# Kernel optimization log

Hardware: AMD Instinct MI355X
Metric: run time of the kernel (lower is better)

Reference implementation:

```python
import jax, jax.numpy as jnp
import numpy as np

D = 768
N_TASKS = 4


def setup_inputs() -> dict:
    key = jax.random.key(0)
    k1, k2, k3, k4, k5 = jax.random.split(key, 5)
    b, s, t = 8, 1024, 1024
    source_features = jax.random.normal(k1, (b, s, D), dtype=jnp.float32)
    target_features = jax.random.normal(k2, (b, t, D), dtype=jnp.float32)
    # learned params: nn.Linear(768,1) + Sigmoid, nn.Embedding(4,768), alpha
    W_cost = jax.random.normal(k3, (D, 1), dtype=jnp.float32) / np.sqrt(D)
    b_cost = jnp.zeros((1,), dtype=jnp.float32)
    task_emb = jax.random.normal(k4, (N_TASKS, D), dtype=jnp.float32)
    alpha = jnp.float32(0.05)
    return {
        "source_features": source_features,
        "target_features": target_features,
        "W_cost": W_cost,
        "b_cost": b_cost,
        "task_emb": task_emb,
        "alpha": alpha,
        "task_id": 2,
    }


def reference(source_features, target_features, W_cost, b_cost, task_emb, alpha, task_id):
    # metric='cosine': elementwise cos of the raw dot-product matrix (as in source)
    dots = jnp.einsum("bsd,btd->bst", source_features, target_features)
    cost = (1.0 - jnp.cos(dots)) / 2.0  # [b,s,t]

    # use_kernel_cost=True: gaussian kernel with h = 1 * std (unbiased, over last two dims)
    std = jnp.std(cost, axis=(-1, -2), keepdims=True, ddof=1)
    cost = jnp.exp(-((cost / std) ** 2) / 2.0)

    # train_cost_matrix=True: conditional MLP on (src + tgt + task_fea), Linear(768,1)+Sigmoid.
    # Linear is applied before the nonlinearity, so decompose to avoid the [b,s,t,768] tensor.
    s_proj = jnp.einsum("bsd,d->bs", source_features, W_cost[:, 0])  # [b,s]
    t_proj = jnp.einsum("btd,d->bt", target_features, W_cost[:, 0])  # [b,t]
    task_proj = jnp.dot(task_emb[task_id], W_cost[:, 0])  # scalar
    cond = jax.nn.sigmoid(
        s_proj[:, :, None] + t_proj[:, None, :] + task_proj + b_cost[0]
    )  # [b,s,t]

    cost = alpha * (cost + cond)
    return cost
```

## Files before the change

### kernel.cpp

```cpp
#include <hip/hip_runtime.h>
#include <hip/hip_bf16.h>
#include <math.h>

#define BATCHES 8
#define SEQ 1024
#define DDIM 768
#define NPANEL 16
#define NK64 12
#define CHUNK_B 8192
#define NK32 24
#define QMAX 6.35f

typedef unsigned short u16;
typedef __attribute__((ext_vector_type(8))) short bf16x8;
typedef __attribute__((ext_vector_type(8))) unsigned short u16x8;
typedef __attribute__((ext_vector_type(4))) float f32x4;
typedef __attribute__((ext_vector_type(4))) int i32x4;

static __device__ __forceinline__ u16 f2bf(float x) {
    union { float f; unsigned u; } v; v.f = x;
    unsigned r = v.u + 0x7FFFu + ((v.u >> 16) & 1u);
    return (u16)(r >> 16);
}
static __device__ __forceinline__ float bf2f(u16 h) {
    union { float f; unsigned u; } v; v.u = ((unsigned)h) << 16; return v.f;
}

__global__ __launch_bounds__(256) void prep_i8(
    const float* __restrict__ S, const float* __restrict__ T,
    const float* __restrict__ W, const float* __restrict__ bcost,
    const float* __restrict__ temb, const int* __restrict__ task_id,
    unsigned char* __restrict__ Sg, unsigned char* __restrict__ Tg,
    float* __restrict__ sproj, float* __restrict__ tproj,
    float* __restrict__ cterm)
{
    int t = threadIdx.x;
    int g = blockIdx.x * 256 + t;
    int r  = g & 15;
    int kg = (g >> 4) & 3;
    int m  = (g >> 6) & 3;
    int x  = g >> 8;
    int ks = x % NK64;
    int y  = x / NK64;
    int p  = y & 15;
    int b  = (y >> 4) & 7;
    int tensor = y >> 7;

    int row_loc = p * 64 + m * 16 + r;
    int row_glb = b * SEQ + row_loc;
    int col = ks * 64 + kg * 16;

    const float* src = (tensor ? T : S) + (size_t)row_glb * DDIM + col;
    float4 f0 = *(const float4*)(src);
    float4 f1 = *(const float4*)(src + 4);
    float4 f2 = *(const float4*)(src + 8);
    float4 f3 = *(const float4*)(src + 12);
    float4 w0 = *(const float4*)(W + col);
    float4 w1 = *(const float4*)(W + col + 4);
    float4 w2 = *(const float4*)(W + col + 8);
    float4 w3 = *(const float4*)(W + col + 12);

    float xv[16] = {f0.x,f0.y,f0.z,f0.w, f1.x,f1.y,f1.z,f1.w,
                    f2.x,f2.y,f2.z,f2.w, f3.x,f3.y,f3.z,f3.w};
    float wv[16] = {w0.x,w0.y,w0.z,w0.w, w1.x,w1.y,w1.z,w1.w,
                    w2.x,w2.y,w2.z,w2.w, w3.x,w3.y,w3.z,w3.w};

    float pd = 0.f;
    #pragma unroll
    for (int e = 0; e < 16; ++e) pd = fmaf(xv[e], wv[e], pd);
    pd += __shfl_down(pd, 32);
    pd += __shfl_down(pd, 16);
    if ((t & 63) < 16)
        atomicAdd((tensor ? tproj : sproj) + row_glb, pd);

    const float s     = QMAX / 127.0f;
    const float inv_s = 127.0f / QMAX;
    const float inv_s2 = 252.0f / s;
    unsigned q1w[4] = {0,0,0,0}, q2w[4] = {0,0,0,0};
    #pragma unroll
    for (int e = 0; e < 16; ++e) {
        float v = xv[e];
        float q1f = rintf(v * inv_s);
        q1f = fminf(fmaxf(q1f, -127.f), 127.f);
        float rr = fmaf(-q1f, s, v);
        float q2f = rintf(rr * inv_s2);
        q2f = fminf(fmaxf(q2f, -126.f), 126.f);
        unsigned b1 = (unsigned)(unsigned char)(char)(int)q1f;
        unsigned b2 = (unsigned)(unsigned char)(char)(int)q2f;
        q1w[e >> 2] |= b1 << ((e & 3) * 8);
        q2w[e >> 2] |= b2 << ((e & 3) * 8);
    }
    unsigned char* dst = (tensor ? Tg : Sg)
        + (size_t)((b * NPANEL + p) * NK64 + ks) * CHUNK_B
        + (m * 1024 + kg * 256 + r * 16);
    *(uint4*)dst          = (uint4){q1w[0], q1w[1], q1w[2], q1w[3]};
    *(uint4*)(dst + 4096) = (uint4){q2w[0], q2w[1], q2w[2], q2w[3]};

    if (blockIdx.x == 0 && t < 64) {
        int tid = *task_id;
        float sacc = 0.f;
        #pragma unroll
        for (int d = t; d < DDIM; d += 64) sacc = fmaf(temb[tid * DDIM + d], W[d], sacc);
        #pragma unroll
        for (int o = 32; o; o >>= 1) sacc += __shfl_down(sacc, o);
        if (t == 0) *cterm = sacc + bcost[0];
    }
}

__global__ __launch_bounds__(256) void proj_kernel(
    const float* __restrict__ S, const float* __restrict__ T,
    const float* __restrict__ W, const float* __restrict__ bcost,
    const float* __restrict__ temb, const int* __restrict__ task_id,
    float* __restrict__ sproj, float* __restrict__ tproj,
    float* __restrict__ cterm)
{
    int gw   = (blockIdx.x * blockDim.x + threadIdx.x) >> 6;
    int lane = threadIdx.x & 63;

    if (gw < 2 * BATCHES * SEQ) {
        const float* rowp = (gw < BATCHES * SEQ)
            ? S + (size_t)gw * DDIM
            : T + (size_t)(gw - BATCHES * SEQ) * DDIM;
        float s = 0.f;
        #pragma unroll
        for (int d = lane; d < DDIM; d += 64) s = fmaf(rowp[d], W[d], s);
        #pragma unroll
        for (int o = 32; o; o >>= 1) s += __shfl_down(s, o);
        if (lane == 0) {
            if (gw < BATCHES * SEQ) sproj[gw] = s;
            else                    tproj[gw - BATCHES * SEQ] = s;
        }
    }
    if (blockIdx.x == gridDim.x - 1 && (threadIdx.x >> 6) == 0) {
        int tid = *task_id;
        float s = 0.f;
        #pragma unroll
        for (int d = lane; d < DDIM; d += 64) s = fmaf(temb[tid * DDIM + d], W[d], s);
        #pragma unroll
        for (int o = 32; o; o >>= 1) s += __shfl_down(s, o);
        if (lane == 0) *cterm = s + bcost[0];
    }
}

__global__ __launch_bounds__(256, 2) void gemm_i8(
    const unsigned char* __restrict__ Sg, const unsigned char* __restrict__ Tg,
    float* __restrict__ out, double* __restrict__ batch_sums)
{
    __shared__ double red[8];

    const int t    = threadIdx.x;
    const int lane = t & 63;
    const int w    = t >> 6;

    int swz  = ((blockIdx.x & 7) << 6) + (blockIdx.x >> 3);
    int tile = swz * 4 + w;
    const int b  = tile >> 8;
    const int by = (tile >> 4) & 15;
    const int bx = tile & 15;

    i32x4 acc_hh[4][4], acc_x[4][4];
    #pragma unroll
    for (int m = 0; m < 4; ++m)
        #pragma unroll
        for (int n = 0; n < 4; ++n) {
            acc_hh[m][n] = (i32x4){0,0,0,0};
            acc_x[m][n]  = (i32x4){0,0,0,0};
        }

    const unsigned char* Achunk = Sg + (size_t)((b * NPANEL + by) * NK64) * CHUNK_B + lane * 16;
    const unsigned char* Bchunk = Tg + (size_t)((b * NPANEL + bx) * NK64) * CHUNK_B + lane * 16;

    #pragma unroll 1
    for (int ks = 0; ks < NK64; ++ks) {
        const unsigned char* Ak = Achunk + (size_t)ks * CHUNK_B;
        const unsigned char* Bk = Bchunk + (size_t)ks * CHUNK_B;
        i32x4 a1[4], a2[4], b1[4], b2[4];
        #pragma unroll
        for (int m = 0; m < 4; ++m) {
            a1[m] = *(const i32x4*)(Ak + m * 1024);
            a2[m] = *(const i32x4*)(Ak + 4096 + m * 1024);
        }
        #pragma unroll
        for (int n = 0; n < 4; ++n) {
            b1[n] = *(const i32x4*)(Bk + n * 1024);
            b2[n] = *(const i32x4*)(Bk + 4096 + n * 1024);
        }
        #pragma unroll
        for (int m = 0; m < 4; ++m)
            #pragma unroll
            for (int n = 0; n < 4; ++n) {
                acc_hh[m][n] = __builtin_amdgcn_mfma_i32_16x16x64_i8(a1[m], b1[n], acc_hh[m][n], 0, 0, 0);
                acc_x[m][n]  = __builtin_amdgcn_mfma_i32_16x16x64_i8(a1[m], b2[n], acc_x[m][n], 0, 0, 0);
                acc_x[m][n]  = __builtin_amdgcn_mfma_i32_16x16x64_i8(a2[m], b1[n], acc_x[m][n], 0, 0, 0);
            }
    }

    const float S2  = (QMAX / 127.0f) * (QMAX / 127.0f);
    const float S2F = S2 / 252.0f;
    float lsum = 0.f, lsq = 0.f;
    float* outb = out + (size_t)b * SEQ * SEQ;
    const int rbase = by * 64;
    const int cbase = bx * 64;
    const int cr = lane >> 4;
    const int cc = lane & 15;
    #pragma unroll
    for (int m = 0; m < 4; ++m) {
        #pragma unroll
        for (int n = 0; n < 4; ++n) {
            int col = cbase + n * 16 + cc;
            #pragma unroll
            for (int j = 0; j < 4; ++j) {
                int row = rbase + m * 16 + cr * 4 + j;
                float d  = S2 * (float)acc_hh[m][n][j] + S2F * (float)acc_x[m][n][j];
                float c0 = 0.5f - 0.5f * __cosf(d);
                outb[(size_t)row * SEQ + col] = c0;
                lsum += c0;
                lsq  = fmaf(c0, c0, lsq);
            }
        }
    }

    double s = (double)lsum, q = (double)lsq;
    #pragma unroll
    for (int o = 32; o; o >>= 1) { s += __shfl_down(s, o); q += __shfl_down(q, o); }
    if (lane == 0) { red[w] = s; red[4 + w] = q; }
    __syncthreads();
    if (t == 0) {
        s = red[0] + red[1] + red[2] + red[3];
        q = red[4] + red[5] + red[6] + red[7];
        atomicAdd(&batch_sums[b * 2 + 0], s);
        atomicAdd(&batch_sums[b * 2 + 1], q);
    }
}

__global__ __launch_bounds__(256) void gemm_fused_bf16(
    const float* __restrict__ S, const float* __restrict__ T,
    float* __restrict__ out, double* __restrict__ batch_sums)
{
    __shared__ __align__(16) u16 lds[16384];
    __shared__ double red[8];

    const int t    = threadIdx.x;
    const int lane = t & 63;
    const int w    = t >> 6;
    const int wr   = w >> 1, wc = w & 1;

    int wg = (blockIdx.x & 7) * 64 + (blockIdx.x >> 3);
    const int b  = wg >> 6;
    const int by = (wg >> 3) & 7;
    const int bx = wg & 7;

    f32x4 acc[4][4];
    #pragma unroll
    for (int m = 0; m < 4; ++m)
        #pragma unroll
        for (int n = 0; n < 4; ++n) acc[m][n] = (f32x4){0.f, 0.f, 0.f, 0.f};

    const float* Sb = S + (size_t)b * SEQ * DDIM;
    const float* Tb = T + (size_t)b * SEQ * DDIM;
    const float* pa[2]; const float* pb[2];
    float4 ra[2][2], rb[2][2];
    #pragma unroll
    for (int i = 0; i < 2; ++i) {
        int g = t + i * 256;
        int m = g >> 6, kg = (g >> 4) & 3, r = g & 15;
        pa[i] = Sb + (size_t)(by * 128 + m * 16 + r) * DDIM + kg * 8;
        pb[i] = Tb + (size_t)(bx * 128 + m * 16 + r) * DDIM + kg * 8;
    }

    auto LOADREGS = [&](int ks) {
        #pragma unroll
        for (int i = 0; i < 2; ++i) {
            ra[i][0] = *(const float4*)(pa[i] + ks * 32);
            ra[i][1] = *(const float4*)(pa[i] + ks * 32 + 4);
            rb[i][0] = *(const float4*)(pb[i] + ks * 32);
            rb[i][1] = *(const float4*)(pb[i] + ks * 32 + 4);
        }
    };
    auto STAGE_FUSED = [&]() {
        #pragma unroll
        for (int i = 0; i < 2; ++i) {
            int g = t + i * 256;
            float xa[8] = {ra[i][0].x, ra[i][0].y, ra[i][0].z, ra[i][0].w,
                           ra[i][1].x, ra[i][1].y, ra[i][1].z, ra[i][1].w};
            float xb[8] = {rb[i][0].x, rb[i][0].y, rb[i][0].z, rb[i][0].w,
                           rb[i][1].x, rb[i][1].y, rb[i][1].z, rb[i][1].w};
            u16x8 ah, al, bh, bl;
            #pragma unroll
            for (int e = 0; e < 8; ++e) {
                u16 h = f2bf(xa[e]); ah[e] = h; al[e] = f2bf(xa[e] - bf2f(h));
                u16 g2 = f2bf(xb[e]); bh[e] = g2; bl[e] = f2bf(xb[e] - bf2f(g2));
            }
            *(u16x8*)&lds[(size_t)g * 8]         = ah;
            *(u16x8*)&lds[4096 + (size_t)g * 8]  = al;
            *(u16x8*)&lds[8192 + (size_t)g * 8]  = bh;
            *(u16x8*)&lds[12288 + (size_t)g * 8] = bl;
        }
    };
    auto COMPUTE = [&]() {
        const u16* L = &lds[0];
        bf16x8 ah[4], al[4], bh[4], bl[4];
        #pragma unroll
        for (int m = 0; m < 4; ++m) {
            int sm = wr * 4 + m;
            ah[m] = *(const bf16x8*)(L + sm * 512 + lane * 8);
            al[m] = *(const bf16x8*)(L + 4096 + sm * 512 + lane * 8);
        }
        #pragma unroll
        for (int n = 0; n < 4; ++n) {
            int sn = wc * 4 + n;
            bh[n] = *(const bf16x8*)(L + 8192 + sn * 512 + lane * 8);
            bl[n] = *(const bf16x8*)(L + 12288 + sn * 512 + lane * 8);
        }
        #pragma unroll
        for (int m = 0; m < 4; ++m)
            #pragma unroll
            for (int n = 0; n < 4; ++n) {
                acc[m][n] = __builtin_amdgcn_mfma_f32_16x16x32_bf16(ah[m], bh[n], acc[m][n], 0, 0, 0);
                acc[m][n] = __builtin_amdgcn_mfma_f32_16x16x32_bf16(ah[m], bl[n], acc[m][n], 0, 0, 0);
                acc[m][n] = __builtin_amdgcn_mfma_f32_16x16x32_bf16(al[m], bh[n], acc[m][n], 0, 0, 0);
            }
    };

    LOADREGS(0);
    for (int ks = 0; ks < NK32; ++ks) {
        STAGE_FUSED();
        __syncthreads();
        if (ks + 1 < NK32) LOADREGS(ks + 1);
        COMPUTE();
        __syncthreads();
    }

    float lsum = 0.f, lsq = 0.f;
    float* outb = out + (size_t)b * SEQ * SEQ;
    const int rbase = by * 128 + wr * 64;
    const int cbase = bx * 128 + wc * 64;
    const int cr = lane >> 4;
    const int cc = lane & 15;
    #pragma unroll
    for (int m = 0; m < 4; ++m) {
        #pragma unroll
        for (int n = 0; n < 4; ++n) {
            int col = cbase + n * 16 + cc;
            #pragma unroll
            for (int j = 0; j < 4; ++j) {
                int row = rbase + m * 16 + cr * 4 + j;
                float d  = acc[m][n][j];
                float c0 = 0.5f - 0.5f * __cosf(d);
                outb[(size_t)row * SEQ + col] = c0;
                lsum += c0;
                lsq  = fmaf(c0, c0, lsq);
            }
        }
    }

    double s = (double)lsum, q = (double)lsq;
    #pragma unroll
    for (int o = 32; o; o >>= 1) { s += __shfl_down(s, o); q += __shfl_down(q, o); }
    if (lane == 0) { red[w] = s; red[4 + w] = q; }
    __syncthreads();
    if (t == 0) {
        s = red[0] + red[1] + red[2] + red[3];
        q = red[4] + red[5] + red[6] + red[7];
        atomicAdd(&batch_sums[b * 2 + 0], s);
        atomicAdd(&batch_sums[b * 2 + 1], q);
    }
}

__global__ __launch_bounds__(256) void finalize_kernel(
    float* __restrict__ out, const double* __restrict__ batch_sums,
    const float* __restrict__ sproj, const float* __restrict__ tproj,
    const float* __restrict__ cterm_p, const float* __restrict__ alpha_p)
{
    const double n = (double)SEQ * (double)SEQ;
    size_t idx4 = (size_t)blockIdx.x * blockDim.x + threadIdx.x;
    size_t base = idx4 * 4;
    int batch = (int)(base >> 20);
    int rem   = (int)(base & ((SEQ * SEQ) - 1));
    int srow  = rem >> 10;
    int tcol  = rem & (SEQ - 1);

    double sum = batch_sums[batch * 2 + 0];
    double sq  = batch_sums[batch * 2 + 1];
    double var = (sq - sum * sum / n) / (n - 1.0);
    float inv_std = (float)(1.0 / sqrt(var));

    float alpha = *alpha_p;
    float ct    = *cterm_p;
    float sp    = sproj[batch * SEQ + srow];
    float4 tp   = *(const float4*)&tproj[batch * SEQ + tcol];
    float4 c    = *(float4*)&out[base];

    float4 r;
    { float x = c.x * inv_std; float g = __expf(-0.5f * x * x);
      float z = sp + tp.x + ct; float cd = 1.f / (1.f + __expf(-z)); r.x = alpha * (g + cd); }
    { float x = c.y * inv_std; float g = __expf(-0.5f * x * x);
      float z = sp + tp.y + ct; float cd = 1.f / (1.f + __expf(-z)); r.y = alpha * (g + cd); }
    { float x = c.z * inv_std; float g = __expf(-0.5f * x * x);
      float z = sp + tp.z + ct; float cd = 1.f / (1.f + __expf(-z)); r.z = alpha * (g + cd); }
    { float x = c.w * inv_std; float g = __expf(-0.5f * x * x);
      float z = sp + tp.w + ct; float cd = 1.f / (1.f + __expf(-z)); r.w = alpha * (g + cd); }
    *(float4*)&out[base] = r;
}

extern "C" void kernel_launch(void* const* d_in, const int* in_sizes, int n_in,
                              void* d_out, int out_size, void* d_ws, size_t ws_size,
                              hipStream_t stream) {
    const float* S      = (const float*)d_in[0];
    const float* T      = (const float*)d_in[1];
    const float* W      = (const float*)d_in[2];
    const float* bcost  = (const float*)d_in[3];
    const float* temb   = (const float*)d_in[4];
    const float* alpha  = (const float*)d_in[5];
    const int*   taskid = (const int*)d_in[6];
    float* out = (float*)d_out;

    double* batch_sums = (double*)d_ws;
    float*  sproj = (float*)((char*)d_ws + 128);
    float*  tproj = sproj + BATCHES * SEQ;
    float*  cterm = tproj + BATCHES * SEQ;

    const size_t ZERO_BYTES = 128 + sizeof(float) * (2 * BATCHES * SEQ + 1);
    const size_t SMALL = (size_t)1 << 20;
    const size_t CONV_B = (size_t)BATCHES * NPANEL * NK64 * CHUNK_B;
    const size_t NEEDED = SMALL + 2 * CONV_B;
    unsigned char* Sg = (unsigned char*)d_ws + SMALL;
    unsigned char* Tg = Sg + CONV_B;

    hipMemsetAsync(d_ws, 0, ZERO_BYTES, stream);

    if (ws_size >= NEEDED) {
        int nblk = (2 * BATCHES * NPANEL * NK64 * 256) / 256;
        prep_i8<<<nblk, 256, 0, stream>>>(S, T, W, bcost, temb, taskid,
                                          Sg, Tg, sproj, tproj, cterm);
        gemm_i8<<<512, 256, 0, stream>>>(Sg, Tg, out, batch_sums);
    } else {
        proj_kernel<<<4097, 256, 0, stream>>>(S, T, W, bcost, temb, taskid,
                                              sproj, tproj, cterm);
        gemm_fused_bf16<<<512, 256, 0, stream>>>(S, T, out, batch_sums);
    }

    int nblk2 = (BATCHES * SEQ * SEQ) / (256 * 4);
    finalize_kernel<<<nblk2, 256, 0, stream>>>(out, batch_sums, sproj, tproj,
                                               cterm, alpha);
}
```

Baseline: 66.95 us.

## Store intermediate cosine cost as fp16 and halve per-wave GEMM tile

The int8 GEMM now writes the intermediate (1-cos)/2 values to an fp16 scratch buffer instead of fp32 into the output. A new finalize kernel reads that buffer eight elements at a time, which cuts round-trip memory traffic on the intermediate. Each wave's tile also drops from 64x64 to 32x64, which doubles the grid and raises the occupancy hint to 4. The costs are fp16 rounding of the intermediate before the Gaussian and less operand reuse per wave.

```diff
diff --git a/kernel.cpp b/kernel.cpp
--- a/kernel.cpp
+++ b/kernel.cpp
@@ -142,9 +142,9 @@
     }
 }
 
-__global__ __launch_bounds__(256, 2) void gemm_i8(
+__global__ __launch_bounds__(256, 4) void gemm_i8(
     const unsigned char* __restrict__ Sg, const unsigned char* __restrict__ Tg,
-    float* __restrict__ out, double* __restrict__ batch_sums)
+    _Float16* __restrict__ c0buf, double* __restrict__ batch_sums)
 {
     __shared__ double red[8];
 
@@ -152,31 +152,34 @@
     const int lane = t & 63;
     const int w    = t >> 6;
 
-    int swz  = ((blockIdx.x & 7) << 6) + (blockIdx.x >> 3);
-    int tile = swz * 4 + w;
-    const int b  = tile >> 8;
-    const int by = (tile >> 4) & 15;
-    const int bx = tile & 15;
-
-    i32x4 acc_hh[4][4], acc_x[4][4];
-    #pragma unroll
-    for (int m = 0; m < 4; ++m)
+    const int b   = blockIdx.x & 7;
+    const int q   = blockIdx.x >> 3;
+    const int bx  = q & 15;
+    const int byh = ((q >> 4) << 2) + w;
+    const int p   = byh >> 1;
+    const int h   = byh & 1;
+
+    i32x4 acc_hh[2][4], acc_x[2][4];
+    #pragma unroll
+    for (int m = 0; m < 2; ++m)
         #pragma unroll
         for (int n = 0; n < 4; ++n) {
             acc_hh[m][n] = (i32x4){0,0,0,0};
             acc_x[m][n]  = (i32x4){0,0,0,0};
         }
 
-    const unsigned char* Achunk = Sg + (size_t)((b * NPANEL + by) * NK64) * CHUNK_B + lane * 16;
-    const unsigned char* Bchunk = Tg + (size_t)((b * NPANEL + bx) * NK64) * CHUNK_B + lane * 16;
+    const unsigned char* Achunk = Sg + (size_t)((b * NPANEL + p) * NK64) * CHUNK_B
+                                + (h * 2) * 1024 + lane * 16;
+    const unsigned char* Bchunk = Tg + (size_t)((b * NPANEL + bx) * NK64) * CHUNK_B
+                                + lane * 16;
 
     #pragma unroll 1
     for (int ks = 0; ks < NK64; ++ks) {
         const unsigned char* Ak = Achunk + (size_t)ks * CHUNK_B;
         const unsigned char* Bk = Bchunk + (size_t)ks * CHUNK_B;
-        i32x4 a1[4], a2[4], b1[4], b2[4];
-        #pragma unroll
-        for (int m = 0; m < 4; ++m) {
+        i32x4 a1[2], a2[2], b1[4], b2[4];
+        #pragma unroll
+        for (int m = 0; m < 2; ++m) {
             a1[m] = *(const i32x4*)(Ak + m * 1024);
             a2[m] = *(const i32x4*)(Ak + 4096 + m * 1024);
         }
@@ -186,7 +189,7 @@
             b2[n] = *(const i32x4*)(Bk + 4096 + n * 1024);
         }
         #pragma unroll
-        for (int m = 0; m < 4; ++m)
+        for (int m = 0; m < 2; ++m)
             #pragma unroll
             for (int n = 0; n < 4; ++n) {
                 acc_hh[m][n] = __builtin_amdgcn_mfma_i32_16x16x64_i8(a1[m], b1[n], acc_hh[m][n], 0, 0, 0);
@@ -198,13 +201,13 @@
     const float S2  = (QMAX / 127.0f) * (QMAX / 127.0f);
     const float S2F = S2 / 252.0f;
     float lsum = 0.f, lsq = 0.f;
-    float* outb = out + (size_t)b * SEQ * SEQ;
-    const int rbase = by * 64;
+    _Float16* cb = c0buf + (size_t)b * SEQ * SEQ;
+    const int rbase = byh * 32;
     const int cbase = bx * 64;
     const int cr = lane >> 4;
     const int cc = lane & 15;
     #pragma unroll
-    for (int m = 0; m < 4; ++m) {
+    for (int m = 0; m < 2; ++m) {
         #pragma unroll
         for (int n = 0; n < 4; ++n) {
             int col = cbase + n * 16 + cc;
@@ -213,23 +216,23 @@
                 int row = rbase + m * 16 + cr * 4 + j;
                 float d  = S2 * (float)acc_hh[m][n][j] + S2F * (float)acc_x[m][n][j];
                 float c0 = 0.5f - 0.5f * __cosf(d);
-                outb[(size_t)row * SEQ + col] = c0;
+                cb[(size_t)row * SEQ + col] = (_Float16)c0;
                 lsum += c0;
                 lsq  = fmaf(c0, c0, lsq);
             }
         }
     }
 
-    double s = (double)lsum, q = (double)lsq;
-    #pragma unroll
-    for (int o = 32; o; o >>= 1) { s += __shfl_down(s, o); q += __shfl_down(q, o); }
-    if (lane == 0) { red[w] = s; red[4 + w] = q; }
+    double s = (double)lsum, q2 = (double)lsq;
+    #pragma unroll
+    for (int o = 32; o; o >>= 1) { s += __shfl_down(s, o); q2 += __shfl_down(q2, o); }
+    if (lane == 0) { red[w] = s; red[4 + w] = q2; }
     __syncthreads();
     if (t == 0) {
-        s = red[0] + red[1] + red[2] + red[3];
-        q = red[4] + red[5] + red[6] + red[7];
+        s  = red[0] + red[1] + red[2] + red[3];
+        q2 = red[4] + red[5] + red[6] + red[7];
         atomicAdd(&batch_sums[b * 2 + 0], s);
-        atomicAdd(&batch_sums[b * 2 + 1], q);
+        atomicAdd(&batch_sums[b * 2 + 1], q2);
     }
 }
 
@@ -367,7 +370,48 @@
     }
 }
 
-__global__ __launch_bounds__(256) void finalize_kernel(
+__global__ __launch_bounds__(256) void finalize_half(
+    float* __restrict__ out, const _Float16* __restrict__ c0buf,
+    const double* __restrict__ batch_sums,
+    const float* __restrict__ sproj, const float* __restrict__ tproj,
+    const float* __restrict__ cterm_p, const float* __restrict__ alpha_p)
+{
+    const double n = (double)SEQ * (double)SEQ;
+    size_t idx8 = (size_t)blockIdx.x * blockDim.x + threadIdx.x;
+    size_t base = idx8 * 8;
+    int batch = (int)(base >> 20);
+    int rem   = (int)(base & ((SEQ * SEQ) - 1));
+    int srow  = rem >> 10;
+    int tcol  = rem & (SEQ - 1);
+
+    double sum = batch_sums[batch * 2 + 0];
+    double sq  = batch_sums[batch * 2 + 1];
+    double var = (sq - sum * sum / n) / (n - 1.0);
+    float inv_std = (float)(1.0 / sqrt(var));
+
+    float alpha = *alpha_p;
+    float ct    = *cterm_p;
+    float sp    = sproj[batch * SEQ + srow] + ct;
+    float4 tp0  = *(const float4*)&tproj[batch * SEQ + tcol];
+    float4 tp1  = *(const float4*)&tproj[batch * SEQ + tcol + 4];
+
+    _Float16 h[8];
+    *(uint4*)h = *(const uint4*)(c0buf + base);
+    float tps[8] = {tp0.x, tp0.y, tp0.z, tp0.w, tp1.x, tp1.y, tp1.z, tp1.w};
+    float r[8];
+    #pragma unroll
+    for (int e = 0; e < 8; ++e) {
+        float x = (float)h[e] * inv_std;
+        float g = __expf(-0.5f * x * x);
+        float z = sp + tps[e];
+        float cd = 1.f / (1.f + __expf(-z));
+        r[e] = alpha * (g + cd);
+    }
+    *(float4*)&out[base]     = (float4){r[0], r[1], r[2], r[3]};
+    *(float4*)&out[base + 4] = (float4){r[4], r[5], r[6], r[7]};
+}
+
+__global__ __launch_bounds__(256) void finalize_f32(
     float* __restrict__ out, const double* __restrict__ batch_sums,
     const float* __restrict__ sproj, const float* __restrict__ tproj,
     const float* __restrict__ cterm_p, const float* __restrict__ alpha_p)
@@ -423,9 +467,11 @@
     const size_t ZERO_BYTES = 128 + sizeof(float) * (2 * BATCHES * SEQ + 1);
     const size_t SMALL = (size_t)1 << 20;
     const size_t CONV_B = (size_t)BATCHES * NPANEL * NK64 * CHUNK_B;
-    const size_t NEEDED = SMALL + 2 * CONV_B;
+    const size_t C0_B   = (size_t)BATCHES * SEQ * SEQ * 2;
+    const size_t NEEDED = SMALL + 2 * CONV_B + C0_B;
     unsigned char* Sg = (unsigned char*)d_ws + SMALL;
     unsigned char* Tg = Sg + CONV_B;
+    _Float16* c0buf = (_Float16*)(Tg + CONV_B);
 
     hipMemsetAsync(d_ws, 0, ZERO_BYTES, stream);
 
@@ -433,14 +479,16 @@
         int nblk = (2 * BATCHES * NPANEL * NK64 * 256) / 256;
         prep_i8<<<nblk, 256, 0, stream>>>(S, T, W, bcost, temb, taskid,
                                           Sg, Tg, sproj, tproj, cterm);
-        gemm_i8<<<512, 256, 0, stream>>>(Sg, Tg, out, batch_sums);
+        gemm_i8<<<1024, 256, 0, stream>>>(Sg, Tg, c0buf, batch_sums);
+        int nfin = (BATCHES * SEQ * SEQ) / (256 * 8);
+        finalize_half<<<nfin, 256, 0, stream>>>(out, c0buf, batch_sums,
+                                                sproj, tproj, cterm, alpha);
     } else {
         proj_kernel<<<4097, 256, 0, stream>>>(S, T, W, bcost, temb, taskid,
                                               sproj, tproj, cterm);
         gemm_fused_bf16<<<512, 256, 0, stream>>>(S, T, out, batch_sums);
-    }
-
-    int nblk2 = (BATCHES * SEQ * SEQ) / (256 * 4);
-    finalize_kernel<<<nblk2, 256, 0, stream>>>(out, batch_sums, sproj, tproj,
+        int nfin = (BATCHES * SEQ * SEQ) / (256 * 4);
+        finalize_f32<<<nfin, 256, 0, stream>>>(out, batch_sums, sproj, tproj,
                                                cterm, alpha);
-}
+    }
+}
```

Result: no change. 65.98 us (median of 2 runs) (-1.4%).
